# Performance work log

Measured on AMD Instinct MI355X. Metric: run time of the kernel, lower is better.

Reference implementation:

```python
import jax, jax.numpy as jnp
import numpy as np


def make_coord(h, w):
    # grid-center coords in [-1,1], stacked as (y, x), matching torch make_coord
    y = (2.0 * jnp.arange(h, dtype=jnp.float32) + 1.0) / h - 1.0
    x = (2.0 * jnp.arange(w, dtype=jnp.float32) + 1.0) / w - 1.0
    yy, xx = jnp.meshgrid(y, x, indexing='ij')
    return jnp.stack([yy, xx], axis=-1).reshape(-1, 2)  # [h*w, 2]


def setup_inputs() -> dict:
    key = jax.random.key(0)
    ks = jax.random.split(key, 11)
    N, C, Hf, Wf = 4, 64, 64, 64
    inp = {"img_feature": jax.random.normal(ks[0], (N, C, Hf, Wf), dtype=jnp.float32)}
    dims = [68, 256, 256, 256, 256, 3]  # in_dim = C + 2 (rel_coord) + 2 (rel_cell)
    for i in range(5):
        inp[f"w{i}"] = jax.random.normal(ks[1 + i], (dims[i], dims[i + 1]), dtype=jnp.float32) * (1.0 / np.sqrt(dims[i]))
        inp[f"b{i}"] = jax.random.normal(ks[6 + i], (dims[i + 1],), dtype=jnp.float32) * 0.01
    inp["h"] = 256
    inp["w"] = 256
    inp["cell_scale"] = 1
    inp["bsize"] = 30000
    return inp


def _forward(img_feature, w0, b0, w1, b1, w2, b2, w3, b3, w4, b4, h, w, cell_scale):
    feat = img_feature
    N, C, Hf, Wf = feat.shape
    Q = h * w
    coord = make_coord(h, w)  # [Q, 2] (y, x)
    cell = jnp.stack([
        jnp.full((Q,), 2.0 / (h * cell_scale), dtype=jnp.float32),
        jnp.full((Q,), 2.0 / (w * cell_scale), dtype=jnp.float32),
    ], axis=-1)  # [Q, 2]

    rx = 1.0 / Hf  # = 2 / Hf / 2
    ry = 1.0 / Wf
    eps_shift = 1e-6
    scale = jnp.array([Hf, Wf], dtype=jnp.float32)
    rel_cell = cell * scale  # [Q, 2]

    # features laid out for per-query gather: [N, Hf*Wf, C]
    feat_flat = jnp.transpose(feat, (0, 2, 3, 1)).reshape(N, Hf * Wf, C)

    layers = [(w0, b0), (w1, b1), (w2, b2), (w3, b3), (w4, b4)]

    def mlp(x):
        for wi, bi in layers[:-1]:
            x = jax.nn.relu(x @ wi + bi)
        wl, bl = layers[-1]
        return x @ wl + bl

    preds = []
    areas = []
    for vx in (-1, 1):
        for vy in (-1, 1):
            c = coord + jnp.array([vx * rx + eps_shift, vy * ry + eps_shift], dtype=jnp.float32)
            c = jnp.clip(c, -1.0 + 1e-6, 1.0 - 1e-6)
            # grid_sample nearest, align_corners=False: idx = round(((g+1)*S - 1)/2)
            iy = jnp.clip(jnp.round(((c[:, 0] + 1.0) * Hf - 1.0) * 0.5), 0, Hf - 1).astype(jnp.int32)
            ix = jnp.clip(jnp.round(((c[:, 1] + 1.0) * Wf - 1.0) * 0.5), 0, Wf - 1).astype(jnp.int32)
            idx = iy * Wf + ix  # [Q]
            q_feat = feat_flat[:, idx, :]  # [N, Q, C] irregular gather
            # nearest feature-grid center coords (same values grid_sample of feat_coord returns)
            q_coord = jnp.stack([
                (2.0 * iy.astype(jnp.float32) + 1.0) / Hf - 1.0,
                (2.0 * ix.astype(jnp.float32) + 1.0) / Wf - 1.0,
            ], axis=-1)  # [Q, 2]
            rel = (coord - q_coord) * scale  # [Q, 2]
            x = jnp.concatenate([
                q_feat,
                jnp.broadcast_to(rel[None], (N, Q, 2)),
                jnp.broadcast_to(rel_cell[None], (N, Q, 2)),
            ], axis=-1)  # [N, Q, 68]
            preds.append(mlp(x))  # [N, Q, 3]
            areas.append(jnp.abs(rel[:, 0] * rel[:, 1]) + 1e-9)  # [Q]

    tot_area = areas[0] + areas[1] + areas[2] + areas[3]
    # local-ensemble swap: 0<->3, 1<->2 (opposite-corner weighting)
    areas = [areas[3], areas[2], areas[1], areas[0]]
    ret = jnp.zeros((N, Q, 3), dtype=jnp.float32)
    for p, a in zip(preds, areas):
        ret = ret + p * (a / tot_area)[None, :, None]
    return jnp.transpose(ret.reshape(N, h, w, 3), (0, 3, 1, 2))  # [N, 3, h, w]


def reference(img_feature, w0, b0, w1, b1, w2, b2, w3, b3, w4, b4, h, w, cell_scale, bsize):
    # bsize only chunks the query loop in the original; math is identical without chunking
    return _forward(img_feature, w0, b0, w1, b1, w2, b2, w3, b3, w4, b4, h, w, cell_scale)
```

## Files before the change

kernel.cpp:

```cpp
#include <hip/hip_runtime.h>


typedef _Float16 f16;
typedef _Float16 f16x8 __attribute__((ext_vector_type(8)));
typedef _Float16 f16x4 __attribute__((ext_vector_type(4)));
typedef float    f32x4 __attribute__((ext_vector_type(4)));

#define MFMA(a, b, c) __builtin_amdgcn_mfma_f32_16x16x32_f16((a), (b), (c), 0, 0, 0)

constexpr int HF = 64, WF = 64;
constexpr int HO = 256, WO = 256;
constexpr int Q = HO * WO;
constexpr int D = 256;
constexpr int K0P = 96;
constexpr int STR = 264;
constexpr int R = 128;

constexpr size_t OFF_FEAT = 0;
constexpr size_t OFF_W0   = 2097152;
constexpr size_t OFF_W1   = OFF_W0 + 256 * 96 * 2;
constexpr size_t OFF_W2   = OFF_W1 + 256 * 256 * 2;
constexpr size_t OFF_W3   = OFF_W2 + 256 * 256 * 2;
constexpr size_t OFF_W4   = OFF_W3 + 256 * 256 * 2;

__global__ void prep_feat(const float* __restrict__ f, f16* __restrict__ ft) {
  int idx = blockIdx.x * 256 + threadIdx.x;
  int c = idx & 63, p = (idx >> 6) & 4095, n = idx >> 18;
  ft[idx] = (f16)f[((((size_t)n << 6) | c) << 12) | p];
}

__global__ void prep_w(const float* __restrict__ w, f16* __restrict__ wt,
                       int K, int N, int Kpad, int Npad) {
  int idx = blockIdx.x * 256 + threadIdx.x;
  if (idx >= Npad * Kpad) return;
  int k = idx % Kpad, n = idx / Kpad;
  wt[idx] = (f16)((k < K && n < N) ? w[k * N + n] : 0.0f);
}

__device__ __forceinline__ void tap_geom(int q, float vx, float vy,
                                         int& p, float& rel0, float& rel1) {
  int qy = q >> 8, qx = q & (WO - 1);
  float cy0 = (float)(2 * qy + 1) * (1.0f / HO) - 1.0f;
  float cx0 = (float)(2 * qx + 1) * (1.0f / WO) - 1.0f;
  float cy = cy0 + vx * (1.0f / HF) + 1e-6f;
  float cx = cx0 + vy * (1.0f / WF) + 1e-6f;
  cy = fminf(fmaxf(cy, -1.0f + 1e-6f), 1.0f - 1e-6f);
  cx = fminf(fmaxf(cx, -1.0f + 1e-6f), 1.0f - 1e-6f);
  int iy = (int)rintf(((cy + 1.0f) * (float)HF - 1.0f) * 0.5f);
  int ix = (int)rintf(((cx + 1.0f) * (float)WF - 1.0f) * 0.5f);
  iy = min(max(iy, 0), HF - 1);
  ix = min(max(ix, 0), WF - 1);
  p = (iy << 6) | ix;
  rel0 = (cy0 - ((float)(2 * iy + 1) * (1.0f / HF) - 1.0f)) * (float)HF;
  rel1 = (cx0 - ((float)(2 * ix + 1) * (1.0f / WF) - 1.0f)) * (float)WF;
}

__device__ __forceinline__ float blend_wt(int q, int t) {
  float a[4], tot = 0.0f;
#pragma unroll
  for (int u = 0; u < 4; ++u) {
    int p; float r0, r1;
    tap_geom(q, (u & 2) ? 1.0f : -1.0f, (u & 1) ? 1.0f : -1.0f, p, r0, r1);
    a[u] = fabsf(r0 * r1) + 1e-9f;
    tot += a[u];
  }
  float sel = (t == 0) ? a[3] : (t == 1) ? a[2] : (t == 2) ? a[1] : a[0];
  return sel / tot;
}

template <int KSTEPS, int KPAD>
__device__ __forceinline__ void mlp_layer(f16* X, const f16* __restrict__ wt,
                                          const float* __restrict__ bv,
                                          int wv, int col, int quad) {
  f32x4 acc[4][8];
#pragma unroll
  for (int mt = 0; mt < 4; ++mt)
#pragma unroll
    for (int nt = 0; nt < 8; ++nt) acc[mt][nt] = 0.0f;

  const f16* ap = wt + (wv * 64 + col) * KPAD + quad * 8;
  const f16* bp = X + col * STR + quad * 8;
#pragma unroll 1
  for (int s = 0; s < KSTEPS; ++s) {
    f16x8 b[8];
#pragma unroll
    for (int nt = 0; nt < 8; ++nt)
      b[nt] = *(const f16x8*)(bp + s * 32 + nt * 16 * STR);
#pragma unroll
    for (int mt = 0; mt < 4; ++mt) {
      f16x8 a = *(const f16x8*)(ap + s * 32 + mt * 16 * KPAD);
#pragma unroll
      for (int nt = 0; nt < 8; ++nt) acc[mt][nt] = MFMA(a, b[nt], acc[mt][nt]);
    }
  }
  __syncthreads();
#pragma unroll
  for (int mt = 0; mt < 4; ++mt) {
    float4 bb = *(const float4*)(bv + wv * 64 + mt * 16 + quad * 4);
#pragma unroll
    for (int nt = 0; nt < 8; ++nt) {
      f16x4 y;
      y[0] = (f16)fmaxf(acc[mt][nt][0] + bb.x, 0.0f);
      y[1] = (f16)fmaxf(acc[mt][nt][1] + bb.y, 0.0f);
      y[2] = (f16)fmaxf(acc[mt][nt][2] + bb.z, 0.0f);
      y[3] = (f16)fmaxf(acc[mt][nt][3] + bb.w, 0.0f);
      *(f16x4*)(X + (nt * 16 + col) * STR + wv * 64 + mt * 16 + quad * 4) = y;
    }
  }
  __syncthreads();
}

__global__ __launch_bounds__(256, 2) void liif_main(
    const f16* __restrict__ featT,
    const f16* __restrict__ wt0, const f16* __restrict__ wt1,
    const f16* __restrict__ wt2, const f16* __restrict__ wt3,
    const f16* __restrict__ wt4,
    const float* __restrict__ b0, const float* __restrict__ b1,
    const float* __restrict__ b2, const float* __restrict__ b3,
    const float* __restrict__ b4, float* __restrict__ out) {
  __shared__ __attribute__((aligned(16))) f16 X[R * STR];
  const int tid = threadIdx.x;
  const int wv = tid >> 6;
  const int lane = tid & 63;
  const int row0 = blockIdx.x * R;
  const int n = row0 >> 16;
  const int q0 = row0 & (Q - 1);
  const int col = lane & 15, quad = lane >> 4;

  float oacc[2][4] = {{0, 0, 0, 0}, {0, 0, 0, 0}};
  float bias4[4];
#pragma unroll
  for (int i = 0; i < 4; ++i) bias4[i] = (i < 3) ? b4[i] : 0.0f;

#pragma unroll 1
  for (int t = 0; t < 4; ++t) {
    const float vx = (t & 2) ? 1.0f : -1.0f;
    const float vy = (t & 1) ? 1.0f : -1.0f;

    __syncthreads();
    {
      const int gr = tid >> 1, hf = tid & 1;
      int p; float r0, r1;
      tap_geom(q0 + gr, vx, vy, p, r0, r1);
      const f16x8* src = (const f16x8*)(featT + (((size_t)n << 12) + p) * 64 + hf * 32);
      f16x8* dst = (f16x8*)(X + gr * STR + hf * 32);
      dst[0] = src[0]; dst[1] = src[1]; dst[2] = src[2]; dst[3] = src[3];
      if (tid < R) {
        int p2; float s0, s1;
        tap_geom(q0 + tid, vx, vy, p2, s0, s1);
        f16* xr = X + tid * STR;
        f16x4 relv = {(f16)s0, (f16)s1, (f16)0.5f, (f16)0.5f};
        *(f16x4*)(xr + 64) = relv;
        f16x4 z4 = {0, 0, 0, 0};
        f16x8 z8 = {0, 0, 0, 0, 0, 0, 0, 0};
        *(f16x4*)(xr + 68) = z4;
        *(f16x8*)(xr + 72) = z8;
        *(f16x8*)(xr + 80) = z8;
        *(f16x8*)(xr + 88) = z8;
      }
    }
    __syncthreads();

    mlp_layer<3, K0P>(X, wt0, b0, wv, col, quad);
    mlp_layer<8, D>(X, wt1, b1, wv, col, quad);
    mlp_layer<8, D>(X, wt2, b2, wv, col, quad);
    mlp_layer<8, D>(X, wt3, b3, wv, col, quad);

    f32x4 facc[2];
    facc[0] = 0.0f; facc[1] = 0.0f;
    {
      const f16* ap = wt4 + col * D + quad * 8;
      const f16* bp = X + (wv * 32 + col) * STR + quad * 8;
#pragma unroll 1
      for (int s = 0; s < 8; ++s) {
        f16x8 a = *(const f16x8*)(ap + s * 32);
        f16x8 bq0 = *(const f16x8*)(bp + s * 32);
        f16x8 bq1 = *(const f16x8*)(bp + 16 * STR + s * 32);
        facc[0] = MFMA(a, bq0, facc[0]);
        facc[1] = MFMA(a, bq1, facc[1]);
      }
    }
#pragma unroll
    for (int nt = 0; nt < 2; ++nt) {
      int q = q0 + wv * 32 + nt * 16 + col;
      float w = blend_wt(q, t);
#pragma unroll
      for (int i = 0; i < 4; ++i) oacc[nt][i] += (facc[nt][i] + bias4[i]) * w;
    }
  }

  if (quad == 0) {
#pragma unroll
    for (int nt = 0; nt < 2; ++nt) {
      int q = q0 + wv * 32 + nt * 16 + col;
#pragma unroll
      for (int c = 0; c < 3; ++c)
        out[(((size_t)(n * 3 + c)) << 16) + q] = oacc[nt][c];
    }
  }
}

extern "C" void kernel_launch(void* const* d_in, const int* in_sizes, int n_in,
                              void* d_out, int out_size, void* d_ws, size_t ws_size,
                              hipStream_t stream) {
  const float* feat = (const float*)d_in[0];
  const float* w0 = (const float*)d_in[1];
  const float* b0 = (const float*)d_in[2];
  const float* w1 = (const float*)d_in[3];
  const float* b1 = (const float*)d_in[4];
  const float* w2 = (const float*)d_in[5];
  const float* b2 = (const float*)d_in[6];
  const float* w3 = (const float*)d_in[7];
  const float* b3 = (const float*)d_in[8];
  const float* w4 = (const float*)d_in[9];
  const float* b4 = (const float*)d_in[10];

  char* ws = (char*)d_ws;
  f16* featT = (f16*)(ws + OFF_FEAT);
  f16* wt0 = (f16*)(ws + OFF_W0);
  f16* wt1 = (f16*)(ws + OFF_W1);
  f16* wt2 = (f16*)(ws + OFF_W2);
  f16* wt3 = (f16*)(ws + OFF_W3);
  f16* wt4 = (f16*)(ws + OFF_W4);

  prep_feat<<<4096, 256, 0, stream>>>(feat, featT);
  prep_w<<<(256 * 96 + 255) / 256, 256, 0, stream>>>(w0, wt0, 68, 256, 96, 256);
  prep_w<<<256, 256, 0, stream>>>(w1, wt1, 256, 256, 256, 256);
  prep_w<<<256, 256, 0, stream>>>(w2, wt2, 256, 256, 256, 256);
  prep_w<<<256, 256, 0, stream>>>(w3, wt3, 256, 256, 256, 256);
  prep_w<<<(16 * 256 + 255) / 256, 256, 0, stream>>>(w4, wt4, 256, 3, 256, 16);

  liif_main<<<Q * 4 / R, 256, 0, stream>>>(featT, wt0, wt1, wt2, wt3, wt4,
                                           b0, b1, b2, b3, b4, (float*)d_out);
}
```

Measured before the change: 616.3 us.

## Switch to single-wave blocks computing all features for 32 rows with pipelined loads

Each block becomes one wave that owns 32 query rows and computes all 256 output features of every MLP layer. This removes all __syncthreads barriers, and the smaller LDS tile allows more blocks per CU. The inner K loop is software-pipelined: weight fragments are prefetched in four groups while MFMAs run, with s_setprio raised around the MFMA bursts. In exchange, each wave now streams the full weight matrix per layer for only 32 rows. That cuts weight reuse per load roughly fourfold and raises L2/L1 traffic and accumulator register pressure.

```diff
diff --git a/kernel.cpp b/kernel.cpp
--- a/kernel.cpp
+++ b/kernel.cpp
@@ -14,7 +14,7 @@
 constexpr int D = 256;
 constexpr int K0P = 96;
 constexpr int STR = 264;
-constexpr int R = 128;
+constexpr int RW = 32;
 
 constexpr size_t OFF_FEAT = 0;
 constexpr size_t OFF_W0   = 2097152;
@@ -71,46 +71,88 @@
 template <int KSTEPS, int KPAD>
 __device__ __forceinline__ void mlp_layer(f16* X, const f16* __restrict__ wt,
                                           const float* __restrict__ bv,
-                                          int wv, int col, int quad) {
-  f32x4 acc[4][8];
+                                          int col, int quad) {
+  f32x4 acc[16][2];
+#pragma unroll
+  for (int M = 0; M < 16; ++M) { acc[M][0] = 0.0f; acc[M][1] = 0.0f; }
+
+  const f16* ap = wt + col * KPAD + quad * 8;
+  const f16* bp = X + col * STR + quad * 8;
+
+  f16x8 aP[4], aQ[4], bP[2], bQ[2];
 #pragma unroll
   for (int mt = 0; mt < 4; ++mt)
-#pragma unroll
-    for (int nt = 0; nt < 8; ++nt) acc[mt][nt] = 0.0f;
-
-  const f16* ap = wt + (wv * 64 + col) * KPAD + quad * 8;
-  const f16* bp = X + col * STR + quad * 8;
+    aP[mt] = *(const f16x8*)(ap + mt * 16 * KPAD);
+  bP[0] = *(const f16x8*)(bp);
+  bP[1] = *(const f16x8*)(bp + 16 * STR);
+
 #pragma unroll 1
   for (int s = 0; s < KSTEPS; ++s) {
-    f16x8 b[8];
-#pragma unroll
-    for (int nt = 0; nt < 8; ++nt)
-      b[nt] = *(const f16x8*)(bp + s * 32 + nt * 16 * STR);
-#pragma unroll
-    for (int mt = 0; mt < 4; ++mt) {
-      f16x8 a = *(const f16x8*)(ap + s * 32 + mt * 16 * KPAD);
-#pragma unroll
-      for (int nt = 0; nt < 8; ++nt) acc[mt][nt] = MFMA(a, b[nt], acc[mt][nt]);
-    }
-  }
-  __syncthreads();
-#pragma unroll
-  for (int mt = 0; mt < 4; ++mt) {
-    float4 bb = *(const float4*)(bv + wv * 64 + mt * 16 + quad * 4);
-#pragma unroll
-    for (int nt = 0; nt < 8; ++nt) {
+#pragma unroll
+    for (int mt = 0; mt < 4; ++mt)
+      aQ[mt] = *(const f16x8*)(ap + (4 + mt) * 16 * KPAD + s * 32);
+    __builtin_amdgcn_s_setprio(1);
+#pragma unroll
+    for (int mt = 0; mt < 4; ++mt) {
+      acc[mt][0] = MFMA(aP[mt], bP[0], acc[mt][0]);
+      acc[mt][1] = MFMA(aP[mt], bP[1], acc[mt][1]);
+    }
+    __builtin_amdgcn_s_setprio(0);
+#pragma unroll
+    for (int mt = 0; mt < 4; ++mt)
+      aP[mt] = *(const f16x8*)(ap + (8 + mt) * 16 * KPAD + s * 32);
+    __builtin_amdgcn_s_setprio(1);
+#pragma unroll
+    for (int mt = 0; mt < 4; ++mt) {
+      acc[4 + mt][0] = MFMA(aQ[mt], bP[0], acc[4 + mt][0]);
+      acc[4 + mt][1] = MFMA(aQ[mt], bP[1], acc[4 + mt][1]);
+    }
+    __builtin_amdgcn_s_setprio(0);
+#pragma unroll
+    for (int mt = 0; mt < 4; ++mt)
+      aQ[mt] = *(const f16x8*)(ap + (12 + mt) * 16 * KPAD + s * 32);
+    if (s + 1 < KSTEPS) {
+      bQ[0] = *(const f16x8*)(bp + (s + 1) * 32);
+      bQ[1] = *(const f16x8*)(bp + 16 * STR + (s + 1) * 32);
+    }
+    __builtin_amdgcn_s_setprio(1);
+#pragma unroll
+    for (int mt = 0; mt < 4; ++mt) {
+      acc[8 + mt][0] = MFMA(aP[mt], bP[0], acc[8 + mt][0]);
+      acc[8 + mt][1] = MFMA(aP[mt], bP[1], acc[8 + mt][1]);
+    }
+    __builtin_amdgcn_s_setprio(0);
+    if (s + 1 < KSTEPS) {
+#pragma unroll
+      for (int mt = 0; mt < 4; ++mt)
+        aP[mt] = *(const f16x8*)(ap + mt * 16 * KPAD + (s + 1) * 32);
+    }
+    __builtin_amdgcn_s_setprio(1);
+#pragma unroll
+    for (int mt = 0; mt < 4; ++mt) {
+      acc[12 + mt][0] = MFMA(aQ[mt], bP[0], acc[12 + mt][0]);
+      acc[12 + mt][1] = MFMA(aQ[mt], bP[1], acc[12 + mt][1]);
+    }
+    __builtin_amdgcn_s_setprio(0);
+    if (s + 1 < KSTEPS) { bP[0] = bQ[0]; bP[1] = bQ[1]; }
+  }
+
+#pragma unroll
+  for (int M = 0; M < 16; ++M) {
+    float4 bb = *(const float4*)(bv + M * 16 + quad * 4);
+#pragma unroll
+    for (int nt = 0; nt < 2; ++nt) {
       f16x4 y;
-      y[0] = (f16)fmaxf(acc[mt][nt][0] + bb.x, 0.0f);
-      y[1] = (f16)fmaxf(acc[mt][nt][1] + bb.y, 0.0f);
-      y[2] = (f16)fmaxf(acc[mt][nt][2] + bb.z, 0.0f);
-      y[3] = (f16)fmaxf(acc[mt][nt][3] + bb.w, 0.0f);
-      *(f16x4*)(X + (nt * 16 + col) * STR + wv * 64 + mt * 16 + quad * 4) = y;
-    }
-  }
-  __syncthreads();
-}
-
-__global__ __launch_bounds__(256, 2) void liif_main(
+      y[0] = (f16)fmaxf(acc[M][nt][0] + bb.x, 0.0f);
+      y[1] = (f16)fmaxf(acc[M][nt][1] + bb.y, 0.0f);
+      y[2] = (f16)fmaxf(acc[M][nt][2] + bb.z, 0.0f);
+      y[3] = (f16)fmaxf(acc[M][nt][3] + bb.w, 0.0f);
+      *(f16x4*)(X + (nt * 16 + col) * STR + M * 16 + quad * 4) = y;
+    }
+  }
+}
+
+__global__ __launch_bounds__(64, 2) void liif_main(
     const f16* __restrict__ featT,
     const f16* __restrict__ wt0, const f16* __restrict__ wt1,
     const f16* __restrict__ wt2, const f16* __restrict__ wt3,
@@ -118,11 +160,9 @@
     const float* __restrict__ b0, const float* __restrict__ b1,
     const float* __restrict__ b2, const float* __restrict__ b3,
     const float* __restrict__ b4, float* __restrict__ out) {
-  __shared__ __attribute__((aligned(16))) f16 X[R * STR];
-  const int tid = threadIdx.x;
-  const int wv = tid >> 6;
-  const int lane = tid & 63;
-  const int row0 = blockIdx.x * R;
+  __shared__ __attribute__((aligned(16))) f16 X[RW * STR];
+  const int lane = threadIdx.x;
+  const int row0 = blockIdx.x * RW;
   const int n = row0 >> 16;
   const int q0 = row0 & (Q - 1);
   const int col = lane & 15, quad = lane >> 4;
@@ -137,18 +177,17 @@
     const float vx = (t & 2) ? 1.0f : -1.0f;
     const float vy = (t & 1) ? 1.0f : -1.0f;
 
-    __syncthreads();
     {
-      const int gr = tid >> 1, hf = tid & 1;
+      const int gr = lane >> 1, hf = lane & 1;
       int p; float r0, r1;
       tap_geom(q0 + gr, vx, vy, p, r0, r1);
       const f16x8* src = (const f16x8*)(featT + (((size_t)n << 12) + p) * 64 + hf * 32);
       f16x8* dst = (f16x8*)(X + gr * STR + hf * 32);
       dst[0] = src[0]; dst[1] = src[1]; dst[2] = src[2]; dst[3] = src[3];
-      if (tid < R) {
+      if (lane < RW) {
         int p2; float s0, s1;
-        tap_geom(q0 + tid, vx, vy, p2, s0, s1);
-        f16* xr = X + tid * STR;
+        tap_geom(q0 + lane, vx, vy, p2, s0, s1);
+        f16* xr = X + lane * STR;
         f16x4 relv = {(f16)s0, (f16)s1, (f16)0.5f, (f16)0.5f};
         *(f16x4*)(xr + 64) = relv;
         f16x4 z4 = {0, 0, 0, 0};
@@ -159,18 +198,17 @@
         *(f16x8*)(xr + 88) = z8;
       }
     }
-    __syncthreads();
-
-    mlp_layer<3, K0P>(X, wt0, b0, wv, col, quad);
-    mlp_layer<8, D>(X, wt1, b1, wv, col, quad);
-    mlp_layer<8, D>(X, wt2, b2, wv, col, quad);
-    mlp_layer<8, D>(X, wt3, b3, wv, col, quad);
+
+    mlp_layer<3, K0P>(X, wt0, b0, col, quad);
+    mlp_layer<8, D>(X, wt1, b1, col, quad);
+    mlp_layer<8, D>(X, wt2, b2, col, quad);
+    mlp_layer<8, D>(X, wt3, b3, col, quad);
 
     f32x4 facc[2];
     facc[0] = 0.0f; facc[1] = 0.0f;
     {
       const f16* ap = wt4 + col * D + quad * 8;
-      const f16* bp = X + (wv * 32 + col) * STR + quad * 8;
+      const f16* bp = X + col * STR + quad * 8;
 #pragma unroll 1
       for (int s = 0; s < 8; ++s) {
         f16x8 a = *(const f16x8*)(ap + s * 32);
@@ -182,7 +220,7 @@
     }
 #pragma unroll
     for (int nt = 0; nt < 2; ++nt) {
-      int q = q0 + wv * 32 + nt * 16 + col;
+      int q = q0 + nt * 16 + col;
       float w = blend_wt(q, t);
 #pragma unroll
       for (int i = 0; i < 4; ++i) oacc[nt][i] += (facc[nt][i] + bias4[i]) * w;
@@ -192,7 +230,7 @@
   if (quad == 0) {
 #pragma unroll
     for (int nt = 0; nt < 2; ++nt) {
-      int q = q0 + wv * 32 + nt * 16 + col;
+      int q = q0 + nt * 16 + col;
 #pragma unroll
       for (int c = 0; c < 3; ++c)
         out[(((size_t)(n * 3 + c)) << 16) + q] = oacc[nt][c];
@@ -230,6 +268,6 @@
   prep_w<<<256, 256, 0, stream>>>(w3, wt3, 256, 256, 256, 256);
   prep_w<<<(16 * 256 + 255) / 256, 256, 0, stream>>>(w4, wt4, 256, 3, 256, 16);
 
-  liif_main<<<Q * 4 / R, 256, 0, stream>>>(featT, wt0, wt1, wt2, wt3, wt4,
+  liif_main<<<Q * 4 / RW, 64, 0, stream>>>(featT, wt0, wt1, wt2, wt3, wt4,
                                            b0, b1, b2, b3, b4, (float*)d_out);
 }
```

After: 1.881 ms. +205.3%, slower.
